# Performance work log

Hardware: AMD Instinct MI355X
Metric: run time of the kernel (lower is better)

The kernel has to match this reference:

```python
import jax, jax.numpy as jnp
import numpy as np

B, C, D, H = 2, 1024, 1024, 16
DH = D // H
EPS = 1e-8


def setup_inputs() -> dict:
    key = jax.random.key(0)
    ks = jax.random.split(key, 12)
    s = 0.02
    return {
        "x": jax.random.normal(ks[0], (B, C, D), dtype=jnp.float32),
        "rms_w": jnp.ones((C, D), dtype=jnp.float32),
        "rms_b": jnp.zeros((C, D), dtype=jnp.float32),
        "Wqkv": jax.random.normal(ks[1], (3 * D, D), dtype=jnp.float32) * s,
        "Wout": jax.random.normal(ks[2], (D, D), dtype=jnp.float32) * s,
        "bout": jnp.zeros((D,), dtype=jnp.float32),
        "Wf": jax.random.normal(ks[3], (D, D), dtype=jnp.float32) * s,
        "bf": jnp.zeros((D,), dtype=jnp.float32),
        "Ww": jax.random.normal(ks[4], (D, D), dtype=jnp.float32) * s,
        "bw": jnp.zeros((D,), dtype=jnp.float32),
        "Wv": jax.random.normal(ks[5], (D, D), dtype=jnp.float32) * s,
        "bv": jnp.zeros((D,), dtype=jnp.float32),
        "beta": jnp.ones((1,), dtype=jnp.float32),
    }


def _rope_cos_sin(C, dh):
    # faithful to source: theta = 10000 ** (-2*(i-1)/dh), i in [0, dh//2)
    i = jnp.arange(dh // 2, dtype=jnp.float32)
    theta = 10000.0 ** (-2.0 * (i - 1.0) / dh)            # [dh//2]
    ang = jnp.arange(C, dtype=jnp.float32)[:, None] * theta  # [C, dh//2]
    return jnp.cos(ang), jnp.sin(ang)


def _rotate(t, cos, sin):
    # equivalent to einsum('bhci,cij->bhcj', t, R) with the source R
    ev, od = t[..., 0::2], t[..., 1::2]          # [B,H,C,dh//2]
    out_ev = ev * cos + od * sin
    out_od = -ev * sin + od * cos
    return jnp.stack([out_ev, out_od], axis=-1).reshape(t.shape)


def _rmsnorm(x, w, b):
    rms = jnp.sqrt(jnp.mean(x * x, axis=-1, keepdims=True) + EPS)
    return w * (x / rms) + b


def _attention(x, Wqkv, Wout, bout):
    qkv = x @ Wqkv.T                               # [B,C,3D]
    q, k, v = jnp.split(qkv, 3, axis=-1)
    def heads(t):
        return t.reshape(B, C, H, DH).transpose(0, 2, 1, 3)  # [B,H,C,dh]
    q, k, v = heads(q), heads(k), heads(v)
    cos, sin = _rope_cos_sin(C, DH)
    qr = _rotate(q, cos, sin)
    kr = _rotate(k, cos, sin)
    scale = 1.0 / jnp.sqrt(jnp.float32(DH))
    num = jnp.exp(jnp.einsum('bhid,bhjd->bhij', qr, kr) * scale)
    den = jnp.sum(jnp.exp(jnp.einsum('bhid,bhjd->bhij', q, k) * scale),
                  axis=-1, keepdims=True)
    attn = num / den
    mask = jnp.tril(jnp.ones((C, C), dtype=bool))
    attn = jnp.where(mask[None, None], attn, 0.0)
    y = attn @ v                                   # [B,H,C,dh]
    y = y.transpose(0, 2, 1, 3).reshape(B, C, D)
    return y @ Wout.T + bout


def _ffn(x, Wf, bf, Ww, bw, Wv, bv, beta):
    h = x @ Wf.T + bf
    wx = h @ Ww.T + bw
    swish = wx * jax.nn.sigmoid(beta * wx)
    return swish * (h @ Wv.T + bv)


def reference(x, rms_w, rms_b, Wqkv, Wout, bout, Wf, bf, Ww, bw, Wv, bv, beta):
    # dropout p is identity in eval mode
    x = _rmsnorm(x, rms_w, rms_b)
    x = x + _attention(x, Wqkv, Wout, bout)
    x = _rmsnorm(x, rms_w, rms_b)   # same shared RMSNorm module applied twice
    x = x + _ffn(x, Wf, bf, Ww, bw, Wv, bv, beta)
    return x
```

## Files before the change

kernel.cpp:

```cpp
#include <hip/hip_runtime.h>
#include <math.h>

#define B_ 2
#define C_ 1024
#define D_ 1024
#define H_ 16
#define DH_ 64
#define EPSF 1e-8f
#define BK 32

typedef __bf16 bf16;
typedef __attribute__((ext_vector_type(4))) __bf16 bf16x4;
typedef __attribute__((ext_vector_type(8))) __bf16 bf16x8;
typedef __attribute__((ext_vector_type(4))) float f32x4;

__device__ inline f32x4 mfma16(bf16x8 a, bf16x8 b, f32x4 c) {
  return __builtin_amdgcn_mfma_f32_16x16x32_bf16(a, b, c, 0, 0, 0);
}

__device__ inline void async16(const bf16* g, bf16* l) {
  __builtin_amdgcn_global_load_lds((const __attribute__((address_space(1))) void*)g,
                                   (__attribute__((address_space(3))) void*)l, 16, 0, 0);
}

__device__ inline float rope_theta(float i) {
  return exp2f(-13.287712379549449f * (2.0f * (i - 1.0f) * (1.0f / 64.0f)));
}

__global__ __launch_bounds__(256) void cvt_rms_kernel(const float* __restrict__ wqkv,
                                                      const float* __restrict__ wout,
                                                      const float* __restrict__ wf,
                                                      const float* __restrict__ www,
                                                      const float* __restrict__ wv,
                                                      bf16* __restrict__ wdst,
                                                      const float* __restrict__ x,
                                                      const float* __restrict__ rw,
                                                      const float* __restrict__ rb,
                                                      bf16* __restrict__ xout) {
  __shared__ float red[4];
  int t = threadIdx.x;
  if (blockIdx.x < 7 * 1024) {
    int seg = blockIdx.x >> 10;
    int local = (blockIdx.x & 1023) * 1024 + t * 4;
    const float* src = seg < 3 ? wqkv + (size_t)seg * (D_ * D_)
                     : seg == 3 ? wout : seg == 4 ? wf : seg == 5 ? www : wv;
    float4 v = *(const float4*)(src + local);
    bf16x4 o;
    o[0] = (bf16)v.x; o[1] = (bf16)v.y; o[2] = (bf16)v.z; o[3] = (bf16)v.w;
    *(bf16x4*)(wdst + (size_t)seg * (D_ * D_) + local) = o;
    return;
  }
  int row = blockIdx.x - 7 * 1024;
  int c = row & (C_ - 1);
  float4 xv = *(const float4*)(x + (size_t)row * D_ + t * 4);
  float ss = xv.x * xv.x + xv.y * xv.y + xv.z * xv.z + xv.w * xv.w;
#pragma unroll
  for (int m = 1; m < 64; m <<= 1) ss += __shfl_xor(ss, m, 64);
  if ((t & 63) == 0) red[t >> 6] = ss;
  __syncthreads();
  float tot = red[0] + red[1] + red[2] + red[3];
  float inv = rsqrtf(tot * (1.0f / D_) + EPSF);
  float4 wv4 = *(const float4*)(rw + (size_t)c * D_ + t * 4);
  float4 bv4 = *(const float4*)(rb + (size_t)c * D_ + t * 4);
  bf16x4 ov;
  ov[0] = (bf16)(wv4.x * (xv.x * inv) + bv4.x);
  ov[1] = (bf16)(wv4.y * (xv.y * inv) + bv4.y);
  ov[2] = (bf16)(wv4.z * (xv.z * inv) + bv4.z);
  ov[3] = (bf16)(wv4.w * (xv.w * inv) + bv4.w);
  *(bf16x4*)(xout + (size_t)row * D_ + t * 4) = ov;
}

__global__ __launch_bounds__(256) void rmsnorm_bf16_kernel(const bf16* __restrict__ x,
                                                           const float* __restrict__ w,
                                                           const float* __restrict__ b,
                                                           bf16* __restrict__ out) {
  int row = blockIdx.x;
  int c = row & (C_ - 1);
  int t = threadIdx.x;
  bf16x4 xv = *(const bf16x4*)(x + (size_t)row * D_ + t * 4);
  float f0 = (float)xv[0], f1 = (float)xv[1], f2 = (float)xv[2], f3 = (float)xv[3];
  float ss = f0 * f0 + f1 * f1 + f2 * f2 + f3 * f3;
#pragma unroll
  for (int m = 1; m < 64; m <<= 1) ss += __shfl_xor(ss, m, 64);
  __shared__ float red[4];
  if ((t & 63) == 0) red[t >> 6] = ss;
  __syncthreads();
  float tot = red[0] + red[1] + red[2] + red[3];
  float inv = rsqrtf(tot * (1.0f / D_) + EPSF);
  float4 wv = *(const float4*)(w + (size_t)c * D_ + t * 4);
  float4 bv = *(const float4*)(b + (size_t)c * D_ + t * 4);
  bf16x4 ov;
  ov[0] = (bf16)(wv.x * (f0 * inv) + bv.x);
  ov[1] = (bf16)(wv.y * (f1 * inv) + bv.y);
  ov[2] = (bf16)(wv.z * (f2 * inv) + bv.z);
  ov[3] = (bf16)(wv.w * (f3 * inv) + bv.w);
  *(bf16x4*)(out + (size_t)row * D_ + t * 4) = ov;
}

template <int BMt, int BNt>
__global__ __launch_bounds__(256) void gemm_lds(const bf16* __restrict__ A,
                                                const bf16* __restrict__ W,
                                                const float* __restrict__ bias,
                                                const bf16* __restrict__ R,
                                                bf16* __restrict__ Cout,
                                                int M, int N, int K) {
  constexpr int MT = BMt / 32;
  constexpr int NT = BNt / 32;
  __shared__ bf16 sa[BMt * BK];
  __shared__ bf16 sb[BNt * BK];
  int t = threadIdx.x, l = t & 63, w = t >> 6;
  int m0 = blockIdx.y * BMt;
  int n0 = blockIdx.x * BNt;
  int wm = (w >> 1) * (BMt / 2), wn = (w & 1) * (BNt / 2);
  int lm = l & 15, lq = l >> 4;
  f32x4 acc[MT][NT] = {};

  for (int k0 = 0; k0 < K; k0 += BK) {
    __syncthreads();
#pragma unroll
    for (int p = 0; p < BMt / 64; ++p) {
      int lin = p * 256 + t;
      async16(A + (size_t)(m0 + (lin >> 2)) * K + k0 + (lin & 3) * 8, sa + lin * 8);
    }
#pragma unroll
    for (int p = 0; p < BNt / 64; ++p) {
      int lin = p * 256 + t;
      async16(W + (size_t)(n0 + (lin >> 2)) * K + k0 + (lin & 3) * 8, sb + lin * 8);
    }
    __syncthreads();
    bf16x8 af[MT], bfr[NT];
#pragma unroll
    for (int mt = 0; mt < MT; ++mt)
      af[mt] = *(const bf16x8*)(sa + (wm + mt * 16 + lm) * BK + lq * 8);
#pragma unroll
    for (int nt = 0; nt < NT; ++nt)
      bfr[nt] = *(const bf16x8*)(sb + (wn + nt * 16 + lm) * BK + lq * 8);
#pragma unroll
    for (int mt = 0; mt < MT; ++mt)
#pragma unroll
      for (int nt = 0; nt < NT; ++nt)
        acc[mt][nt] = mfma16(af[mt], bfr[nt], acc[mt][nt]);
  }
#pragma unroll
  for (int mt = 0; mt < MT; ++mt)
#pragma unroll
    for (int nt = 0; nt < NT; ++nt) {
      int col = n0 + wn + nt * 16 + lm;
      float bb = bias ? bias[col] : 0.0f;
#pragma unroll
      for (int r = 0; r < 4; ++r) {
        int row = m0 + wm + mt * 16 + lq * 4 + r;
        float v = acc[mt][nt][r] + bb;
        if (R) v += (float)R[(size_t)row * N + col];
        Cout[(size_t)row * N + col] = (bf16)v;
      }
    }
}

__global__ __launch_bounds__(256) void gemm_ffn_kernel(const bf16* __restrict__ A,
                                                       const bf16* __restrict__ Ww,
                                                       const bf16* __restrict__ Wv,
                                                       const float* __restrict__ bw,
                                                       const float* __restrict__ bv,
                                                       const bf16* __restrict__ x3,
                                                       const float* __restrict__ beta_p,
                                                       float* __restrict__ out) {
  __shared__ bf16 sa[64 * BK];
  __shared__ bf16 sb1[64 * BK];
  __shared__ bf16 sb2[64 * BK];
  int t = threadIdx.x, l = t & 63, w = t >> 6;
  int m0 = blockIdx.y * 64, n0 = blockIdx.x * 64;
  int wm = (w >> 1) * 32, wn = (w & 1) * 32;
  int lm = l & 15, lq = l >> 4;
  float beta = beta_p[0];
  f32x4 acc1[2][2] = {}, acc2[2][2] = {};

  for (int k0 = 0; k0 < D_; k0 += BK) {
    __syncthreads();
    async16(A + (size_t)(m0 + (t >> 2)) * D_ + k0 + (t & 3) * 8, sa + t * 8);
    async16(Ww + (size_t)(n0 + (t >> 2)) * D_ + k0 + (t & 3) * 8, sb1 + t * 8);
    async16(Wv + (size_t)(n0 + (t >> 2)) * D_ + k0 + (t & 3) * 8, sb2 + t * 8);
    __syncthreads();
    bf16x8 af[2], b1f[2], b2f[2];
#pragma unroll
    for (int mt = 0; mt < 2; ++mt)
      af[mt] = *(const bf16x8*)(sa + (wm + mt * 16 + lm) * BK + lq * 8);
#pragma unroll
    for (int nt = 0; nt < 2; ++nt) {
      b1f[nt] = *(const bf16x8*)(sb1 + (wn + nt * 16 + lm) * BK + lq * 8);
      b2f[nt] = *(const bf16x8*)(sb2 + (wn + nt * 16 + lm) * BK + lq * 8);
    }
#pragma unroll
    for (int mt = 0; mt < 2; ++mt)
#pragma unroll
      for (int nt = 0; nt < 2; ++nt) {
        acc1[mt][nt] = mfma16(af[mt], b1f[nt], acc1[mt][nt]);
        acc2[mt][nt] = mfma16(af[mt], b2f[nt], acc2[mt][nt]);
      }
  }
#pragma unroll
  for (int mt = 0; mt < 2; ++mt)
#pragma unroll
    for (int nt = 0; nt < 2; ++nt) {
      int col = n0 + wn + nt * 16 + lm;
      float bbw = bw[col], bbv = bv[col];
#pragma unroll
      for (int r = 0; r < 4; ++r) {
        int row = m0 + wm + mt * 16 + lq * 4 + r;
        float z = acc1[mt][nt][r] + bbw;
        float g = acc2[mt][nt][r] + bbv;
        float sw = z / (1.0f + __expf(-beta * z));
        out[(size_t)row * D_ + col] = (float)x3[(size_t)row * D_ + col] + sw * g;
      }
    }
}

__global__ __launch_bounds__(256) void transpose_v_kernel(const bf16* __restrict__ qkv,
                                                          bf16* __restrict__ vt) {
  __shared__ bf16 tile[64][65];
  int t = threadIdx.x;
  int blk = blockIdx.x;
  int ct = blk & 15;
  int h = (blk >> 4) & 15;
  int b = blk >> 8;
  int c0 = ct * 64;
#pragma unroll
  for (int p = 0; p < 16; ++p) {
    int lin = p * 256 + t;
    int cl = lin >> 6, dh = lin & 63;
    tile[dh][cl] = qkv[(size_t)(b * C_ + c0 + cl) * (3 * D_) + 2 * D_ + h * DH_ + dh];
  }
  __syncthreads();
  size_t vbase = (size_t)((b * H_ + h) * DH_) * C_;
#pragma unroll
  for (int p = 0; p < 16; ++p) {
    int lin = p * 256 + t;
    int dh = lin >> 6, cl = lin & 63;
    vt[vbase + (size_t)dh * C_ + c0 + cl] = tile[dh][cl];
  }
}

__global__ __launch_bounds__(256) void attn_kernel(const bf16* __restrict__ qkv,
                                                   const bf16* __restrict__ vt,
                                                   float* __restrict__ yp,
                                                   float* __restrict__ dp) {
  __shared__ bf16 sk[64 * 72];
  __shared__ bf16 skr[64 * 72];
  __shared__ bf16 sv[64 * 72];
  __shared__ bf16 pl[4][16 * 72];
  int t = threadIdx.x, l = t & 63, w = t >> 6;
  int blk = blockIdx.x;
  int half = blk & 1;
  int it = (blk >> 1) & 15;
  int h = (blk >> 5) & 15;
  int b = blk >> 9;
  int i_base = it * 64 + w * 16;
  int lm = l & 15, lq = l >> 4;
  const float scale = 0.125f;
  int jf = half << 9;

  size_t hq = (size_t)h * DH_;
  size_t qrow = (size_t)(b * C_ + i_base + lm) * (3 * D_) + hq;
  bf16x8 qp[2], qrf[2];
  float cq = (float)(i_base + lm);
#pragma unroll
  for (int kk = 0; kk < 2; ++kk) {
    qp[kk] = *(const bf16x8*)(qkv + qrow + kk * 32 + lq * 8);
#pragma unroll
    for (int j = 0; j < 4; ++j) {
      float ip = (float)(kk * 16 + lq * 4 + j);
      float ang = cq * rope_theta(ip);
      float sv_, cv_;
      __sincosf(ang, &sv_, &cv_);
      float qe = (float)qp[kk][2 * j], qo = (float)qp[kk][2 * j + 1];
      qrf[kk][2 * j] = (bf16)(qe * cv_ + qo * sv_);
      qrf[kk][2 * j + 1] = (bf16)(qo * cv_ - qe * sv_);
    }
  }

  float den[4] = {0.f, 0.f, 0.f, 0.f};
  f32x4 yacc[4] = {};
  int i_max = i_base + 15;
  size_t kbase = (size_t)(b * C_) * (3 * D_) + D_ + hq;
  size_t vtbase = (size_t)((b * H_ + h) * DH_) * C_;
  int sr = t >> 3;
  int sc = (t & 7) * 8;
  float th0 = rope_theta((float)((sc >> 1) + 0));
  float th1 = rope_theta((float)((sc >> 1) + 1));
  float th2 = rope_theta((float)((sc >> 1) + 2));
  float th3 = rope_theta((float)((sc >> 1) + 3));

  int4 pk0, pk1, pv0, pv1;
#define FETCH_TILE(J0)                                                          \
  pk0 = *(const int4*)(qkv + kbase + (size_t)((J0) + sr) * (3 * D_) + sc);      \
  pk1 = *(const int4*)(qkv + kbase + (size_t)((J0) + 32 + sr) * (3 * D_) + sc); \
  pv0 = *(const int4*)(vt + vtbase + (size_t)sr * C_ + (J0) + sc);              \
  pv1 = *(const int4*)(vt + vtbase + (size_t)(32 + sr) * C_ + (J0) + sc);

  FETCH_TILE(jf)

  for (int j0 = jf; j0 < jf + 512; j0 += 64) {
    __syncthreads();
    *(int4*)(sk + sr * 72 + sc) = pk0;
    *(int4*)(sk + (32 + sr) * 72 + sc) = pk1;
    *(int4*)(sv + sr * 72 + sc) = pv0;
    *(int4*)(sv + (32 + sr) * 72 + sc) = pv1;
    {
      bf16x8 k0 = *(bf16x8*)&pk0, k1 = *(bf16x8*)&pk1;
      bf16x8 r0, r1;
      float a, s_, c_;
      float jg0 = (float)(j0 + sr), jg1 = (float)(j0 + 32 + sr);
#define ROT(KV, RV, JG, TH, J)                            \
  a = (JG)*TH;                                            \
  __sincosf(a, &s_, &c_);                                 \
  {                                                       \
    float e = (float)KV[2 * J], o = (float)KV[2 * J + 1]; \
    RV[2 * J] = (bf16)(e * c_ + o * s_);                  \
    RV[2 * J + 1] = (bf16)(o * c_ - e * s_);              \
  }
      ROT(k0, r0, jg0, th0, 0) ROT(k0, r0, jg0, th1, 1)
      ROT(k0, r0, jg0, th2, 2) ROT(k0, r0, jg0, th3, 3)
      ROT(k1, r1, jg1, th0, 0) ROT(k1, r1, jg1, th1, 1)
      ROT(k1, r1, jg1, th2, 2) ROT(k1, r1, jg1, th3, 3)
#undef ROT
      *(int4*)(skr + sr * 72 + sc) = *(int4*)&r0;
      *(int4*)(skr + (32 + sr) * 72 + sc) = *(int4*)&r1;
    }
    __syncthreads();
    if (j0 + 64 < jf + 512) {
      FETCH_TILE(j0 + 64)
    }
#pragma unroll
    for (int js = 0; js < 64; js += 16) {
      bf16x8 kf0 = *(const bf16x8*)(sk + (js + lm) * 72 + lq * 8);
      bf16x8 kf1 = *(const bf16x8*)(sk + (js + lm) * 72 + 32 + lq * 8);
      f32x4 s = {0.f, 0.f, 0.f, 0.f};
      s = mfma16(qp[0], kf0, s);
      s = mfma16(qp[1], kf1, s);
#pragma unroll
      for (int r = 0; r < 4; ++r) den[r] += __expf(s[r] * scale);
    }
    if (j0 <= i_max) {
#pragma unroll
      for (int js = 0; js < 64; js += 16) {
        bf16x8 kf0 = *(const bf16x8*)(skr + (js + lm) * 72 + lq * 8);
        bf16x8 kf1 = *(const bf16x8*)(skr + (js + lm) * 72 + 32 + lq * 8);
        f32x4 s = {0.f, 0.f, 0.f, 0.f};
        s = mfma16(qrf[0], kf0, s);
        s = mfma16(qrf[1], kf1, s);
#pragma unroll
        for (int r = 0; r < 4; ++r) {
          int jg = j0 + js + lm;
          int ig = i_base + lq * 4 + r;
          float p = (jg <= ig) ? __expf(s[r] * scale) : 0.0f;
          pl[w][(lq * 4 + r) * 72 + js + lm] = (bf16)p;
        }
      }
      __builtin_amdgcn_wave_barrier();
      bf16x8 pf0 = *(const bf16x8*)(pl[w] + lm * 72 + lq * 8);
      bf16x8 pf1 = *(const bf16x8*)(pl[w] + lm * 72 + 32 + lq * 8);
#pragma unroll
      for (int tt = 0; tt < 4; ++tt) {
        bf16x8 vf0 = *(const bf16x8*)(sv + (tt * 16 + lm) * 72 + lq * 8);
        bf16x8 vf1 = *(const bf16x8*)(sv + (tt * 16 + lm) * 72 + 32 + lq * 8);
        yacc[tt] = mfma16(pf0, vf0, mfma16(pf1, vf1, yacc[tt]));
      }
      __builtin_amdgcn_wave_barrier();
    }
  }
#undef FETCH_TILE
#pragma unroll
  for (int r = 0; r < 4; ++r) {
    float d = den[r];
    d += __shfl_xor(d, 1, 64);
    d += __shfl_xor(d, 2, 64);
    d += __shfl_xor(d, 4, 64);
    d += __shfl_xor(d, 8, 64);
    if (lm == 0) dp[(size_t)blk * 64 + w * 16 + lq * 4 + r] = d;
  }
  size_t yb = (size_t)blk * 4096;
#pragma unroll
  for (int tt = 0; tt < 4; ++tt)
#pragma unroll
    for (int r = 0; r < 4; ++r)
      yp[yb + (size_t)(w * 16 + lq * 4 + r) * 64 + tt * 16 + lm] = yacc[tt][r];
}

__global__ __launch_bounds__(256) void combine_kernel(const float* __restrict__ yp,
                                                      const float* __restrict__ dp,
                                                      bf16* __restrict__ y) {
  int cb = blockIdx.x;
  int it = cb & 15;
  int h = (cb >> 4) & 15;
  int b = cb >> 8;
  int t = threadIdx.x;
  int row = t >> 2;
  int cg = (t & 3) * 16;
  size_t p0 = (size_t)(cb * 2) * 4096 + (size_t)row * 64 + cg;
  size_t p1 = p0 + 4096;
  float inv = 1.0f / (dp[(size_t)(cb * 2) * 64 + row] + dp[(size_t)(cb * 2 + 1) * 64 + row]);
  bf16x8 o0, o1;
#pragma unroll
  for (int c = 0; c < 8; ++c) o0[c] = (bf16)((yp[p0 + c] + yp[p1 + c]) * inv);
#pragma unroll
  for (int c = 0; c < 8; ++c) o1[c] = (bf16)((yp[p0 + 8 + c] + yp[p1 + 8 + c]) * inv);
  size_t ob = (size_t)(b * C_ + it * 64 + row) * D_ + h * DH_ + cg;
  *(bf16x8*)(y + ob) = o0;
  *(bf16x8*)(y + ob + 8) = o1;
}

extern "C" void kernel_launch(void* const* d_in, const int* in_sizes, int n_in,
                              void* d_out, int out_size, void* d_ws, size_t ws_size,
                              hipStream_t stream) {
  const float* x = (const float*)d_in[0];
  const float* rms_w = (const float*)d_in[1];
  const float* rms_b = (const float*)d_in[2];
  const float* Wqkv = (const float*)d_in[3];
  const float* Wout = (const float*)d_in[4];
  const float* bout = (const float*)d_in[5];
  const float* Wf = (const float*)d_in[6];
  const float* bfp = (const float*)d_in[7];
  const float* Ww = (const float*)d_in[8];
  const float* bw = (const float*)d_in[9];
  const float* Wv = (const float*)d_in[10];
  const float* bv = (const float*)d_in[11];
  const float* beta = (const float*)d_in[12];
  float* out = (float*)d_out;

  bf16* ws = (bf16*)d_ws;
  const size_t DD = (size_t)D_ * D_;
  const size_t MC = (size_t)B_ * C_;
  bf16* wb = ws;
  bf16* x1 = ws + 7 * DD;
  bf16* qkv = ws + 9 * DD;
  bf16* vt = ws + 15 * DD;
  bf16* x2 = ws + 17 * DD;
  bf16* x3 = ws + 19 * DD;
  bf16* hbuf = ws + 21 * DD;
  float* yp = (float*)(ws + 24 * DD);
  float* dp = yp + (size_t)1024 * 4096;
  bf16* y = (bf16*)d_out;

  cvt_rms_kernel<<<7 * 1024 + MC, 256, 0, stream>>>(Wqkv, Wout, Wf, Ww, Wv, wb, x, rms_w,
                                                    rms_b, x1);
  gemm_lds<128, 64><<<dim3(3 * D_ / 64, MC / 128), 256, 0, stream>>>(
      x1, wb, nullptr, nullptr, qkv, MC, 3 * D_, D_);
  transpose_v_kernel<<<B_ * H_ * (C_ / 64), 256, 0, stream>>>(qkv, vt);
  attn_kernel<<<B_ * H_ * 16 * 2, 256, 0, stream>>>(qkv, vt, yp, dp);
  combine_kernel<<<B_ * H_ * 16, 256, 0, stream>>>(yp, dp, y);
  gemm_lds<64, 64><<<dim3(D_ / 64, MC / 64), 256, 0, stream>>>(
      y, wb + 3 * DD, bout, x1, x2, MC, D_, D_);
  rmsnorm_bf16_kernel<<<MC, 256, 0, stream>>>(x2, rms_w, rms_b, x3);
  gemm_lds<64, 64><<<dim3(D_ / 64, MC / 64), 256, 0, stream>>>(
      x3, wb + 4 * DD, bfp, nullptr, hbuf, MC, D_, D_);
  gemm_ffn_kernel<<<dim3(D_ / 64, MC / 64), 256, 0, stream>>>(
      hbuf, wb + 5 * DD, wb + 6 * DD, bw, bv, x3, beta, out);
}
```

Measured before the change: 231.4 us.

## Fuse V transpose into QKV GEMM epilogue, use incremental RoPE rotation, reorder attention blocks

The QKV GEMM now writes its V tiles directly in transposed per-head layout through a shared-memory staging buffer, which removes the separate transpose kernel and its global read and write of V. The attention kernel swaps per-tile sincos calls for an angle-addition recurrence that advances cos and sin by a fixed 64-position step. The attention and combine block index mapping is also reordered so the query tile index is the slowest-varying dimension. The recurrence can build up floating-point drift over the tiles, and the extra LDS buffer in the GEMM may lower occupancy.

```diff
diff --git a/kernel.cpp b/kernel.cpp
--- a/kernel.cpp
+++ b/kernel.cpp
@@ -157,6 +157,81 @@
     }
 }
 
+__global__ __launch_bounds__(256) void gemm_qkv_kernel(const bf16* __restrict__ A,
+                                                       const bf16* __restrict__ W,
+                                                       bf16* __restrict__ qkv,
+                                                       bf16* __restrict__ vt) {
+  constexpr int BMt = 128, BNt = 64, MT = 4, NT = 2;
+  const int N = 3 * D_, K = D_;
+  __shared__ bf16 sa[BMt * BK];
+  __shared__ bf16 sb[BNt * BK];
+  __shared__ bf16 tv[64 * 136];
+  int t = threadIdx.x, l = t & 63, w = t >> 6;
+  int m0 = blockIdx.y * BMt;
+  int n0 = blockIdx.x * BNt;
+  int wm = (w >> 1) * 64, wn = (w & 1) * 32;
+  int lm = l & 15, lq = l >> 4;
+  f32x4 acc[MT][NT] = {};
+
+  for (int k0 = 0; k0 < K; k0 += BK) {
+    __syncthreads();
+#pragma unroll
+    for (int p = 0; p < 2; ++p) {
+      int lin = p * 256 + t;
+      async16(A + (size_t)(m0 + (lin >> 2)) * K + k0 + (lin & 3) * 8, sa + lin * 8);
+    }
+    async16(W + (size_t)(n0 + (t >> 2)) * K + k0 + (t & 3) * 8, sb + t * 8);
+    __syncthreads();
+    bf16x8 af[MT], bfr[NT];
+#pragma unroll
+    for (int mt = 0; mt < MT; ++mt)
+      af[mt] = *(const bf16x8*)(sa + (wm + mt * 16 + lm) * BK + lq * 8);
+#pragma unroll
+    for (int nt = 0; nt < NT; ++nt)
+      bfr[nt] = *(const bf16x8*)(sb + (wn + nt * 16 + lm) * BK + lq * 8);
+#pragma unroll
+    for (int mt = 0; mt < MT; ++mt)
+#pragma unroll
+      for (int nt = 0; nt < NT; ++nt)
+        acc[mt][nt] = mfma16(af[mt], bfr[nt], acc[mt][nt]);
+  }
+  if (n0 < 2 * D_) {
+#pragma unroll
+    for (int mt = 0; mt < MT; ++mt)
+#pragma unroll
+      for (int nt = 0; nt < NT; ++nt) {
+        int col = n0 + wn + nt * 16 + lm;
+#pragma unroll
+        for (int r = 0; r < 4; ++r) {
+          int row = m0 + wm + mt * 16 + lq * 4 + r;
+          qkv[(size_t)row * N + col] = (bf16)acc[mt][nt][r];
+        }
+      }
+  } else {
+#pragma unroll
+    for (int mt = 0; mt < MT; ++mt)
+#pragma unroll
+      for (int nt = 0; nt < NT; ++nt) {
+        int dh = wn + nt * 16 + lm;
+#pragma unroll
+        for (int r = 0; r < 4; ++r)
+          tv[dh * 136 + wm + mt * 16 + lq * 4 + r] = (bf16)acc[mt][nt][r];
+      }
+    __syncthreads();
+    int h = (n0 - 2 * D_) >> 6;
+    int bb = m0 >> 10;
+    int mloc = m0 & 1023;
+    size_t vbase = (size_t)((bb * H_ + h) * DH_) * C_;
+#pragma unroll
+    for (int p = 0; p < 4; ++p) {
+      int lin = p * 256 + t;
+      int dh = lin >> 4;
+      int mm = (lin & 15) * 8;
+      *(int4*)(vt + vbase + (size_t)dh * C_ + mloc + mm) = *(int4*)(tv + dh * 136 + mm);
+    }
+  }
+}
+
 __global__ __launch_bounds__(256) void gemm_ffn_kernel(const bf16* __restrict__ A,
                                                        const bf16* __restrict__ Ww,
                                                        const bf16* __restrict__ Wv,
@@ -215,31 +290,6 @@
     }
 }
 
-__global__ __launch_bounds__(256) void transpose_v_kernel(const bf16* __restrict__ qkv,
-                                                          bf16* __restrict__ vt) {
-  __shared__ bf16 tile[64][65];
-  int t = threadIdx.x;
-  int blk = blockIdx.x;
-  int ct = blk & 15;
-  int h = (blk >> 4) & 15;
-  int b = blk >> 8;
-  int c0 = ct * 64;
-#pragma unroll
-  for (int p = 0; p < 16; ++p) {
-    int lin = p * 256 + t;
-    int cl = lin >> 6, dh = lin & 63;
-    tile[dh][cl] = qkv[(size_t)(b * C_ + c0 + cl) * (3 * D_) + 2 * D_ + h * DH_ + dh];
-  }
-  __syncthreads();
-  size_t vbase = (size_t)((b * H_ + h) * DH_) * C_;
-#pragma unroll
-  for (int p = 0; p < 16; ++p) {
-    int lin = p * 256 + t;
-    int dh = lin >> 6, cl = lin & 63;
-    vt[vbase + (size_t)dh * C_ + c0 + cl] = tile[dh][cl];
-  }
-}
-
 __global__ __launch_bounds__(256) void attn_kernel(const bf16* __restrict__ qkv,
                                                    const bf16* __restrict__ vt,
                                                    float* __restrict__ yp,
@@ -250,10 +300,11 @@
   __shared__ bf16 pl[4][16 * 72];
   int t = threadIdx.x, l = t & 63, w = t >> 6;
   int blk = blockIdx.x;
-  int half = blk & 1;
-  int it = (blk >> 1) & 15;
-  int h = (blk >> 5) & 15;
-  int b = blk >> 9;
+  int it = blk >> 6;
+  int r6 = blk & 63;
+  int b = r6 >> 5;
+  int h = (r6 >> 1) & 15;
+  int half = r6 & 1;
   int i_base = it * 64 + w * 16;
   int lm = l & 15, lq = l >> 4;
   const float scale = 0.125f;
@@ -290,6 +341,22 @@
   float th2 = rope_theta((float)((sc >> 1) + 2));
   float th3 = rope_theta((float)((sc >> 1) + 3));
 
+  float cA0, sA0, cA1, sA1, cA2, sA2, cA3, sA3;
+  float cB0, sB0, cB1, sB1, cB2, sB2, cB3, sB3;
+  float C0, S0, C1, S1, C2, S2, C3, S3;
+#define INITP(P)                                              \
+  {                                                           \
+    float a;                                                  \
+    a = (float)(jf + sr) * th##P;                             \
+    __sincosf(a, &sA##P, &cA##P);                             \
+    a = (float)(jf + 32 + sr) * th##P;                        \
+    __sincosf(a, &sB##P, &cB##P);                             \
+    a = 64.0f * th##P;                                        \
+    __sincosf(a, &S##P, &C##P);                               \
+  }
+  INITP(0) INITP(1) INITP(2) INITP(3)
+#undef INITP
+
   int4 pk0, pk1, pv0, pv1;
 #define FETCH_TILE(J0)                                                          \
   pk0 = *(const int4*)(qkv + kbase + (size_t)((J0) + sr) * (3 * D_) + sc);      \
@@ -308,21 +375,26 @@
     {
       bf16x8 k0 = *(bf16x8*)&pk0, k1 = *(bf16x8*)&pk1;
       bf16x8 r0, r1;
-      float a, s_, c_;
-      float jg0 = (float)(j0 + sr), jg1 = (float)(j0 + 32 + sr);
-#define ROT(KV, RV, JG, TH, J)                            \
-  a = (JG)*TH;                                            \
-  __sincosf(a, &s_, &c_);                                 \
+#define ROT2(KV, RV, CC, SS, J)                           \
   {                                                       \
     float e = (float)KV[2 * J], o = (float)KV[2 * J + 1]; \
-    RV[2 * J] = (bf16)(e * c_ + o * s_);                  \
-    RV[2 * J + 1] = (bf16)(o * c_ - e * s_);              \
-  }
-      ROT(k0, r0, jg0, th0, 0) ROT(k0, r0, jg0, th1, 1)
-      ROT(k0, r0, jg0, th2, 2) ROT(k0, r0, jg0, th3, 3)
-      ROT(k1, r1, jg1, th0, 0) ROT(k1, r1, jg1, th1, 1)
-      ROT(k1, r1, jg1, th2, 2) ROT(k1, r1, jg1, th3, 3)
-#undef ROT
+    RV[2 * J] = (bf16)(e * CC + o * SS);                  \
+    RV[2 * J + 1] = (bf16)(o * CC - e * SS);              \
+  }
+      ROT2(k0, r0, cA0, sA0, 0) ROT2(k0, r0, cA1, sA1, 1)
+      ROT2(k0, r0, cA2, sA2, 2) ROT2(k0, r0, cA3, sA3, 3)
+      ROT2(k1, r1, cB0, sB0, 0) ROT2(k1, r1, cB1, sB1, 1)
+      ROT2(k1, r1, cB2, sB2, 2) ROT2(k1, r1, cB3, sB3, 3)
+#undef ROT2
+#define STEP(CX, SX, P)                 \
+  {                                     \
+    float nc = CX * C##P - SX * S##P;   \
+    SX = SX * C##P + CX * S##P;         \
+    CX = nc;                            \
+  }
+      STEP(cA0, sA0, 0) STEP(cA1, sA1, 1) STEP(cA2, sA2, 2) STEP(cA3, sA3, 3)
+      STEP(cB0, sB0, 0) STEP(cB1, sB1, 1) STEP(cB2, sB2, 2) STEP(cB3, sB3, 3)
+#undef STEP
       *(int4*)(skr + sr * 72 + sc) = *(int4*)&r0;
       *(int4*)(skr + (32 + sr) * 72 + sc) = *(int4*)&r1;
     }
@@ -390,9 +462,9 @@
                                                       const float* __restrict__ dp,
                                                       bf16* __restrict__ y) {
   int cb = blockIdx.x;
-  int it = cb & 15;
-  int h = (cb >> 4) & 15;
-  int b = cb >> 8;
+  int it = cb >> 5;
+  int b = (cb >> 4) & 1;
+  int h = cb & 15;
   int t = threadIdx.x;
   int row = t >> 2;
   int cg = (t & 3) * 16;
@@ -443,9 +515,7 @@
 
   cvt_rms_kernel<<<7 * 1024 + MC, 256, 0, stream>>>(Wqkv, Wout, Wf, Ww, Wv, wb, x, rms_w,
                                                     rms_b, x1);
-  gemm_lds<128, 64><<<dim3(3 * D_ / 64, MC / 128), 256, 0, stream>>>(
-      x1, wb, nullptr, nullptr, qkv, MC, 3 * D_, D_);
-  transpose_v_kernel<<<B_ * H_ * (C_ / 64), 256, 0, stream>>>(qkv, vt);
+  gemm_qkv_kernel<<<dim3(3 * D_ / 64, MC / 128), 256, 0, stream>>>(x1, wb, qkv, vt);
   attn_kernel<<<B_ * H_ * 16 * 2, 256, 0, stream>>>(qkv, vt, yp, dp);
   combine_kernel<<<B_ * H_ * 16, 256, 0, stream>>>(yp, dp, y);
   gemm_lds<64, 64><<<dim3(D_ / 64, MC / 64), 256, 0, stream>>>(
```

After: 225.2 us. -2.6%, faster.
